# Kernel optimization log

Measured on AMD Instinct MI355X. Metric: run time of the kernel, lower is better.

The kernel has to match this reference:

```python
import jax, jax.numpy as jnp
import numpy as np

B, S, F, H, W = 16, 2048, 512, 512, 5
PAD = W // 2


def setup_inputs() -> dict:
    key = jax.random.key(0)
    k = jax.random.split(key, 6)
    scale = 0.02
    return {
        "embeds_output": jax.random.normal(k[0], (B, S, F), dtype=jnp.float32),
        "Wq": jax.random.normal(k[1], (F, H), dtype=jnp.float32) * scale,
        "Wk": jax.random.normal(k[2], (F, H), dtype=jnp.float32) * scale,
        "v_att": jax.random.normal(k[3], (H,), dtype=jnp.float32) * scale,
        "cnn_W": jax.random.normal(k[4], (W * F, H), dtype=jnp.float32) * scale,
        "cnn_b": jax.random.normal(k[5], (H,), dtype=jnp.float32) * scale,
    }


def reference(embeds_output, Wq, Wk, v_att, cnn_W, cnn_b):
    b, s, f = embeds_output.shape
    # getConvEmbeds: zero-pad and gather W shifted views -> [B, S, W, F]
    xp = jnp.pad(embeds_output, ((0, 0), (PAD, PAD), (0, 0)))
    windows = jnp.stack([xp[:, i:i + s, :] for i in range(W)], axis=2)  # [B,S,W,F]
    entity = windows[:, :, PAD, :]  # center token, [B,S,F]
    # Bahdanau additive attention over the window
    q = jnp.einsum('bsf,fh->bsh', entity, Wq)          # [B,S,H]
    kproj = jnp.einsum('bswf,fh->bswh', windows, Wk)   # [B,S,W,H]
    scores = jnp.einsum('bswh,h->bsw', jnp.tanh(kproj + q[:, :, None, :]), v_att)
    att = jax.nn.softmax(scores, axis=-1)              # [B,S,W]
    # weight contexts, flatten window dim (row-major W*F, matching torch reshape)
    att_context = (att[..., None] * windows).reshape(b, s, W * F)
    return att_context @ cnn_W + cnn_b                 # [B,S,H]
```

## Files before the change

### kernel.cpp

```cpp
#include <hip/hip_runtime.h>
#include <stdint.h>
#include <stddef.h>

typedef unsigned short u16;
typedef __attribute__((ext_vector_type(8))) short s16x8;
typedef __attribute__((ext_vector_type(8))) unsigned short u16x8;
typedef __attribute__((ext_vector_type(4))) unsigned short u16x4;
typedef __attribute__((ext_vector_type(4))) float f32x4;

typedef __attribute__((address_space(3))) void* as3_void_p;
typedef const __attribute__((address_space(1))) void* as1_cvoid_p;

#define GLD16(gp, lp) __builtin_amdgcn_global_load_lds((as1_cvoid_p)(gp), (as3_void_p)(lp), 16, 0, 0)

enum {
  NS = 2048, NF = 512, NH = 512, NW = 5,
  NROW = 32768,
  K2 = NW * NF
};

__device__ __forceinline__ u16 f2bf(float f) {
  unsigned u = __float_as_uint(f);
  u += 0x7FFFu + ((u >> 16) & 1u);
  return (u16)(u >> 16);
}
__device__ __forceinline__ float bf2f(u16 v) {
  return __uint_as_float(((unsigned)v) << 16);
}


__global__ __launch_bounds__(256) void cvtX(const float* __restrict__ X, u16* __restrict__ Xb) {
  int i = blockIdx.x * 256 + threadIdx.x;
  f32x4 v = ((const f32x4*)X)[i];
  u16x4 o;
  o.x = f2bf(v.x); o.y = f2bf(v.y); o.z = f2bf(v.z); o.w = f2bf(v.w);
  ((u16x4*)Xb)[i] = o;
}

__global__ __launch_bounds__(256) void cvtW(const float* __restrict__ Wq, const float* __restrict__ Wk,
                                            const float* __restrict__ cnnW,
                                            u16* __restrict__ Wt1, u16* __restrict__ Wt2) {
  int i = blockIdx.x * 256 + threadIdx.x;
  if (i < 1024 * 512) {
    int j = i >> 9, f = i & 511;
    float v = (j < 512) ? Wq[(size_t)f * 512 + j] : Wk[(size_t)f * 512 + (j - 512)];
    Wt1[i] = f2bf(v);
  } else {
    int t = i - 1024 * 512;
    int h = t / K2, k = t % K2;
    Wt2[t] = f2bf(cnnW[(size_t)k * 512 + h]);
  }
}


__global__ __launch_bounds__(256) void gemm_qk(const u16* __restrict__ Xb,
                                               const u16* __restrict__ Wt1,
                                               u16* __restrict__ QKb) {
  __shared__ u16 As[128 * 64];
  __shared__ u16 Bs[128 * 64];
  const int tid  = threadIdx.x;
  const int lane = tid & 63, wid = tid >> 6;
  const int wr = wid >> 1, wc = wid & 1;
  const int fr = lane & 15, fq = lane >> 4;
  const int wgid = (blockIdx.x & 7) * 256 + (blockIdx.x >> 3);
  const int brow = (wgid >> 3) * 128;
  const int bcol = (wgid & 7) * 128;

  f32x4 acc[4][4] = {};

  for (int kt = 0; kt < 8; ++kt) {
#pragma unroll
    for (int p = 0; p < 4; ++p) {
      int off = (p * 256 + tid) * 16;
      int r = off >> 7;
      int cb = (off & 127) ^ ((r & 7) << 4);
      const u16* ga = Xb  + (size_t)(brow + r) * NF + kt * 64 + (cb >> 1);
      const u16* gb = Wt1 + (size_t)(bcol + r) * NF + kt * 64 + (cb >> 1);
      GLD16(ga, (char*)As + off);
      GLD16(gb, (char*)Bs + off);
    }
    __syncthreads();
#pragma unroll
    for (int kk = 0; kk < 2; ++kk) {
      s16x8 af[4], bfr[4];
#pragma unroll
      for (int m = 0; m < 4; ++m) {
        int row = wr * 64 + m * 16 + fr;
        af[m] = *(const s16x8*)((const char*)As + row * 128 + ((kk * 64 + fq * 16) ^ ((row & 7) << 4)));
      }
#pragma unroll
      for (int n = 0; n < 4; ++n) {
        int row = wc * 64 + n * 16 + fr;
        bfr[n] = *(const s16x8*)((const char*)Bs + row * 128 + ((kk * 64 + fq * 16) ^ ((row & 7) << 4)));
      }
#pragma unroll
      for (int m = 0; m < 4; ++m)
#pragma unroll
        for (int n = 0; n < 4; ++n)
          acc[m][n] = __builtin_amdgcn_mfma_f32_16x16x32_bf16(af[m], bfr[n], acc[m][n], 0, 0, 0);
    }
    __syncthreads();
  }

#pragma unroll
  for (int m = 0; m < 4; ++m)
#pragma unroll
    for (int n = 0; n < 4; ++n)
#pragma unroll
      for (int r = 0; r < 4; ++r) {
        int row = brow + wr * 64 + m * 16 + fq * 4 + r;
        int col = bcol + wc * 64 + n * 16 + fr;
        QKb[(size_t)row * 1024 + col] = f2bf(acc[m][n][r]);
      }
}


__global__ __launch_bounds__(256) void scores_att(const u16* __restrict__ QKb,
                                                  const float* __restrict__ vatt,
                                                  float* __restrict__ att) {
  const int lane = threadIdx.x & 63;
  const int wid  = threadIdx.x >> 6;
  const int n = blockIdx.x * 4 + wid;
  const int s = n & (NS - 1);
  const int h0 = lane * 8;

  u16x8 qv = *(const u16x8*)(QKb + (size_t)n * 1024 + h0);
  f32x4 va0 = *(const f32x4*)(vatt + h0);
  f32x4 va1 = *(const f32x4*)(vatt + h0 + 4);
  float q[8], vv[8];
#pragma unroll
  for (int j = 0; j < 8; ++j) q[j] = bf2f(qv[j]);
  vv[0] = va0.x; vv[1] = va0.y; vv[2] = va0.z; vv[3] = va0.w;
  vv[4] = va1.x; vv[5] = va1.y; vv[6] = va1.z; vv[7] = va1.w;

  float sc[5];
#pragma unroll
  for (int w = 0; w < 5; ++w) {
    int sp = s + w - 2;
    u16x8 kv = {0, 0, 0, 0, 0, 0, 0, 0};
    if (sp >= 0 && sp < NS)
      kv = *(const u16x8*)(QKb + (size_t)(n + w - 2) * 1024 + 512 + h0);
    float acc = 0.f;
#pragma unroll
    for (int j = 0; j < 8; ++j) {
      float x = q[j] + bf2f(kv[j]);
      x = fminf(fmaxf(x, -15.f), 15.f);
      float e = __expf(2.f * x);
      acc += vv[j] * ((e - 1.f) / (e + 1.f));
    }
    sc[w] = acc;
  }
#pragma unroll
  for (int w = 0; w < 5; ++w)
#pragma unroll
    for (int o = 32; o > 0; o >>= 1)
      sc[w] += __shfl_xor(sc[w], o, 64);

  if (lane == 0) {
    float m = sc[0];
#pragma unroll
    for (int w = 1; w < 5; ++w) m = fmaxf(m, sc[w]);
    float e[5], sum = 0.f;
#pragma unroll
    for (int w = 0; w < 5; ++w) { e[w] = __expf(sc[w] - m); sum += e[w]; }
    float inv = 1.f / sum;
#pragma unroll
    for (int w = 0; w < 5; ++w) att[(size_t)n * 5 + w] = e[w] * inv;
  }
}


__global__ __launch_bounds__(512, 4) void gemm_out(const u16* __restrict__ Xb,
                                                   const u16* __restrict__ Wt2,
                                                   const float* __restrict__ att,
                                                   const float* __restrict__ cnnb,
                                                   float* __restrict__ out) {
  __shared__ u16 As[128 * 64];
  __shared__ u16 Bs[128 * 64];
  __shared__ float att_s[128 * 5];
  const int tid  = threadIdx.x;
  const int lane = tid & 63, wid = tid >> 6;
  const int wr = wid >> 2, wc = wid & 3;
  const int fr = lane & 15, fq = lane >> 4;
  const int wgid = (blockIdx.x & 7) * 128 + (blockIdx.x >> 3);
  const int brow = (wgid >> 2) * 128;
  const int bcol = (wgid & 3) * 128;

  if (tid < 128) {
    int s = (brow + tid) & (NS - 1);
#pragma unroll
    for (int w = 0; w < 5; ++w) {
      int sp = s + w - 2;
      att_s[tid * 5 + w] = (sp >= 0 && sp < NS) ? att[(size_t)(brow + tid) * 5 + w] : 0.f;
    }
  }

  const int rsub = tid >> 3;
  const int cb   = (((tid & 7) ^ (rsub & 7)) << 4);
  const int ldsA0 = tid * 16;
  const int ldsA1 = 8192 + tid * 16;
  const int ldsB0 = tid * 16;
  const int ldsB1 = 8192 + tid * 16;
  const char* gB0 = (const char*)(Wt2 + (size_t)(bcol + rsub) * K2) + cb;
  const char* gB1 = (const char*)(Wt2 + (size_t)(bcol + 64 + rsub) * K2) + cb;

  f32x4 acc[4][2] = {};
  f32x4 accOut[4][2] = {};

  for (int w = 0; w < 5; ++w) {
    int g0 = brow + rsub + w - 2;
    int g1 = brow + 64 + rsub + w - 2;
    g0 = g0 < 0 ? 0 : (g0 >= NROW ? NROW - 1 : g0);
    g1 = g1 < 0 ? 0 : (g1 >= NROW ? NROW - 1 : g1);
    const char* gA0 = (const char*)(Xb + (size_t)g0 * NF) + cb;
    const char* gA1 = (const char*)(Xb + (size_t)g1 * NF) + cb;
    const char* gBw0 = gB0 + w * 1024;
    const char* gBw1 = gB1 + w * 1024;

    for (int kt = 0; kt < 8; ++kt) {
      GLD16(gA0  + kt * 128, (char*)As + ldsA0);
      GLD16(gA1  + kt * 128, (char*)As + ldsA1);
      GLD16(gBw0 + kt * 128, (char*)Bs + ldsB0);
      GLD16(gBw1 + kt * 128, (char*)Bs + ldsB1);
      __syncthreads();
#pragma unroll
      for (int kk = 0; kk < 2; ++kk) {
        s16x8 af[4], bfr[2];
#pragma unroll
        for (int m = 0; m < 4; ++m) {
          int row = wr * 64 + m * 16 + fr;
          af[m] = *(const s16x8*)((const char*)As + row * 128 + ((kk * 64 + fq * 16) ^ ((row & 7) << 4)));
        }
#pragma unroll
        for (int n = 0; n < 2; ++n) {
          int row = wc * 32 + n * 16 + fr;
          bfr[n] = *(const s16x8*)((const char*)Bs + row * 128 + ((kk * 64 + fq * 16) ^ ((row & 7) << 4)));
        }
#pragma unroll
        for (int m = 0; m < 4; ++m)
#pragma unroll
          for (int n = 0; n < 2; ++n)
            acc[m][n] = __builtin_amdgcn_mfma_f32_16x16x32_bf16(af[m], bfr[n], acc[m][n], 0, 0, 0);
      }
      __syncthreads();
    }
#pragma unroll
    for (int m = 0; m < 4; ++m) {
      float a0 = att_s[(wr * 64 + m * 16 + fq * 4 + 0) * 5 + w];
      float a1 = att_s[(wr * 64 + m * 16 + fq * 4 + 1) * 5 + w];
      float a2 = att_s[(wr * 64 + m * 16 + fq * 4 + 2) * 5 + w];
      float a3 = att_s[(wr * 64 + m * 16 + fq * 4 + 3) * 5 + w];
#pragma unroll
      for (int n = 0; n < 2; ++n) {
        accOut[m][n][0] += a0 * acc[m][n][0];
        accOut[m][n][1] += a1 * acc[m][n][1];
        accOut[m][n][2] += a2 * acc[m][n][2];
        accOut[m][n][3] += a3 * acc[m][n][3];
        acc[m][n] = f32x4{0.f, 0.f, 0.f, 0.f};
      }
    }
  }

#pragma unroll
  for (int m = 0; m < 4; ++m)
#pragma unroll
    for (int n = 0; n < 2; ++n)
#pragma unroll
      for (int r = 0; r < 4; ++r) {
        int row = brow + wr * 64 + m * 16 + fq * 4 + r;
        int col = bcol + wc * 32 + n * 16 + fr;
        out[(size_t)row * NH + col] = accOut[m][n][r] + cnnb[col];
      }
}


extern "C" void kernel_launch(void* const* d_in, const int* in_sizes, int n_in,
                              void* d_out, int out_size, void* d_ws, size_t ws_size,
                              hipStream_t stream) {
  const float* X    = (const float*)d_in[0];
  const float* Wq   = (const float*)d_in[1];
  const float* Wk   = (const float*)d_in[2];
  const float* vatt = (const float*)d_in[3];
  const float* cnnW = (const float*)d_in[4];
  const float* cnnb = (const float*)d_in[5];
  float* out = (float*)d_out;

  char* ws = (char*)d_ws;
  u16*   Xb  = (u16*)ws;
  u16*   Wt1 = (u16*)(ws + 33554432);
  u16*   Wt2 = (u16*)(ws + 34603008);
  u16*   QKb = (u16*)(ws + 37224448);
  float* att = (float*)(ws + 104333312);

  cvtX<<<dim3(NROW * NF / 4 / 256), dim3(256), 0, stream>>>(X, Xb);
  cvtW<<<dim3((1024 * 512 + 512 * K2) / 256), dim3(256), 0, stream>>>(Wq, Wk, cnnW, Wt1, Wt2);
  gemm_qk<<<dim3(2048), dim3(256), 0, stream>>>(Xb, Wt1, QKb);
  scores_att<<<dim3(NROW / 4), dim3(256), 0, stream>>>(QKb, vatt, att);
  gemm_out<<<dim3(1024), dim3(512), 0, stream>>>(Xb, Wt2, att, cnnb, out);
}
```

Measured before the change: 208.7 us.

## Merge conversion kernels, widen QK GEMM to 512 threads, swizzle scores blocks

Merges the X and weight conversion kernels into a single launch to save one launch and its tail. Reworks the QK GEMM to use 512 threads per 128x128 tile, so each wave holds 4x2 accumulators instead of 4x4 and issues one global-to-LDS load per operand half per k-step. This targets higher occupancy and fewer registers per wave. Also remaps the scores kernel block index with an XCD-style swizzle, which may change L2 locality.

```diff
diff --git a/kernel.cpp b/kernel.cpp
--- a/kernel.cpp
+++ b/kernel.cpp
@@ -16,7 +16,10 @@
 enum {
   NS = 2048, NF = 512, NH = 512, NW = 5,
   NROW = 32768,
-  K2 = NW * NF
+  K2 = NW * NF,
+  XBLOCKS = NROW * NF / 4 / 256,
+  W_ELEMS = 1024 * 512 + 512 * K2,
+  WBLOCKS = (W_ELEMS + 255) / 256
 };
 
 __device__ __forceinline__ u16 f2bf(float f) {
@@ -29,74 +32,82 @@
 }
 
 
-__global__ __launch_bounds__(256) void cvtX(const float* __restrict__ X, u16* __restrict__ Xb) {
-  int i = blockIdx.x * 256 + threadIdx.x;
-  f32x4 v = ((const f32x4*)X)[i];
-  u16x4 o;
-  o.x = f2bf(v.x); o.y = f2bf(v.y); o.z = f2bf(v.z); o.w = f2bf(v.w);
-  ((u16x4*)Xb)[i] = o;
-}
-
-__global__ __launch_bounds__(256) void cvtW(const float* __restrict__ Wq, const float* __restrict__ Wk,
-                                            const float* __restrict__ cnnW,
-                                            u16* __restrict__ Wt1, u16* __restrict__ Wt2) {
-  int i = blockIdx.x * 256 + threadIdx.x;
-  if (i < 1024 * 512) {
-    int j = i >> 9, f = i & 511;
-    float v = (j < 512) ? Wq[(size_t)f * 512 + j] : Wk[(size_t)f * 512 + (j - 512)];
-    Wt1[i] = f2bf(v);
+__global__ __launch_bounds__(256) void cvt_all(const float* __restrict__ X,
+                                               const float* __restrict__ Wq,
+                                               const float* __restrict__ Wk,
+                                               const float* __restrict__ cnnW,
+                                               u16* __restrict__ Xb,
+                                               u16* __restrict__ Wt1,
+                                               u16* __restrict__ Wt2) {
+  int b = blockIdx.x;
+  if (b < XBLOCKS) {
+    int i = b * 256 + threadIdx.x;
+    f32x4 v = ((const f32x4*)X)[i];
+    u16x4 o;
+    o.x = f2bf(v.x); o.y = f2bf(v.y); o.z = f2bf(v.z); o.w = f2bf(v.w);
+    ((u16x4*)Xb)[i] = o;
   } else {
-    int t = i - 1024 * 512;
-    int h = t / K2, k = t % K2;
-    Wt2[t] = f2bf(cnnW[(size_t)k * 512 + h]);
-  }
-}
-
-
-__global__ __launch_bounds__(256) void gemm_qk(const u16* __restrict__ Xb,
-                                               const u16* __restrict__ Wt1,
-                                               u16* __restrict__ QKb) {
+    int i = (b - XBLOCKS) * 256 + threadIdx.x;
+    if (i >= W_ELEMS) return;
+    if (i < 1024 * 512) {
+      int j = i >> 9, f = i & 511;
+      float v = (j < 512) ? Wq[(size_t)f * 512 + j] : Wk[(size_t)f * 512 + (j - 512)];
+      Wt1[i] = f2bf(v);
+    } else {
+      int t = i - 1024 * 512;
+      int h = t / K2, k = t % K2;
+      Wt2[t] = f2bf(cnnW[(size_t)k * 512 + h]);
+    }
+  }
+}
+
+
+__global__ __launch_bounds__(512, 4) void gemm_qk(const u16* __restrict__ Xb,
+                                                  const u16* __restrict__ Wt1,
+                                                  u16* __restrict__ QKb) {
   __shared__ u16 As[128 * 64];
   __shared__ u16 Bs[128 * 64];
   const int tid  = threadIdx.x;
   const int lane = tid & 63, wid = tid >> 6;
-  const int wr = wid >> 1, wc = wid & 1;
+  const int wr = wid >> 2, wc = wid & 3;
   const int fr = lane & 15, fq = lane >> 4;
   const int wgid = (blockIdx.x & 7) * 256 + (blockIdx.x >> 3);
   const int brow = (wgid >> 3) * 128;
   const int bcol = (wgid & 7) * 128;
 
-  f32x4 acc[4][4] = {};
+  const int rsub = tid >> 3;
+  const int cb   = (((tid & 7) ^ (rsub & 7)) << 4);
+  const char* gA0 = (const char*)(Xb  + (size_t)(brow + rsub) * NF) + cb;
+  const char* gA1 = (const char*)(Xb  + (size_t)(brow + 64 + rsub) * NF) + cb;
+  const char* gB0 = (const char*)(Wt1 + (size_t)(bcol + rsub) * NF) + cb;
+  const char* gB1 = (const char*)(Wt1 + (size_t)(bcol + 64 + rsub) * NF) + cb;
+
+  f32x4 acc[4][2] = {};
 
   for (int kt = 0; kt < 8; ++kt) {
-#pragma unroll
-    for (int p = 0; p < 4; ++p) {
-      int off = (p * 256 + tid) * 16;
-      int r = off >> 7;
-      int cb = (off & 127) ^ ((r & 7) << 4);
-      const u16* ga = Xb  + (size_t)(brow + r) * NF + kt * 64 + (cb >> 1);
-      const u16* gb = Wt1 + (size_t)(bcol + r) * NF + kt * 64 + (cb >> 1);
-      GLD16(ga, (char*)As + off);
-      GLD16(gb, (char*)Bs + off);
-    }
+    const int ko = kt * 128;
+    GLD16(gA0 + ko, (char*)As + tid * 16);
+    GLD16(gA1 + ko, (char*)As + 8192 + tid * 16);
+    GLD16(gB0 + ko, (char*)Bs + tid * 16);
+    GLD16(gB1 + ko, (char*)Bs + 8192 + tid * 16);
     __syncthreads();
 #pragma unroll
     for (int kk = 0; kk < 2; ++kk) {
-      s16x8 af[4], bfr[4];
+      s16x8 af[4], bfr[2];
 #pragma unroll
       for (int m = 0; m < 4; ++m) {
         int row = wr * 64 + m * 16 + fr;
         af[m] = *(const s16x8*)((const char*)As + row * 128 + ((kk * 64 + fq * 16) ^ ((row & 7) << 4)));
       }
 #pragma unroll
-      for (int n = 0; n < 4; ++n) {
-        int row = wc * 64 + n * 16 + fr;
+      for (int n = 0; n < 2; ++n) {
+        int row = wc * 32 + n * 16 + fr;
         bfr[n] = *(const s16x8*)((const char*)Bs + row * 128 + ((kk * 64 + fq * 16) ^ ((row & 7) << 4)));
       }
 #pragma unroll
       for (int m = 0; m < 4; ++m)
 #pragma unroll
-        for (int n = 0; n < 4; ++n)
+        for (int n = 0; n < 2; ++n)
           acc[m][n] = __builtin_amdgcn_mfma_f32_16x16x32_bf16(af[m], bfr[n], acc[m][n], 0, 0, 0);
     }
     __syncthreads();
@@ -105,11 +116,11 @@
 #pragma unroll
   for (int m = 0; m < 4; ++m)
 #pragma unroll
-    for (int n = 0; n < 4; ++n)
+    for (int n = 0; n < 2; ++n)
 #pragma unroll
       for (int r = 0; r < 4; ++r) {
         int row = brow + wr * 64 + m * 16 + fq * 4 + r;
-        int col = bcol + wc * 64 + n * 16 + fr;
+        int col = bcol + wc * 32 + n * 16 + fr;
         QKb[(size_t)row * 1024 + col] = f2bf(acc[m][n][r]);
       }
 }
@@ -120,7 +131,8 @@
                                                   float* __restrict__ att) {
   const int lane = threadIdx.x & 63;
   const int wid  = threadIdx.x >> 6;
-  const int n = blockIdx.x * 4 + wid;
+  const int wgid = (blockIdx.x & 7) * 1024 + (blockIdx.x >> 3);
+  const int n = wgid * 4 + wid;
   const int s = n & (NS - 1);
   const int h0 = lane * 8;
 
@@ -197,10 +209,6 @@
 
   const int rsub = tid >> 3;
   const int cb   = (((tid & 7) ^ (rsub & 7)) << 4);
-  const int ldsA0 = tid * 16;
-  const int ldsA1 = 8192 + tid * 16;
-  const int ldsB0 = tid * 16;
-  const int ldsB1 = 8192 + tid * 16;
   const char* gB0 = (const char*)(Wt2 + (size_t)(bcol + rsub) * K2) + cb;
   const char* gB1 = (const char*)(Wt2 + (size_t)(bcol + 64 + rsub) * K2) + cb;
 
@@ -218,10 +226,11 @@
     const char* gBw1 = gB1 + w * 1024;
 
     for (int kt = 0; kt < 8; ++kt) {
-      GLD16(gA0  + kt * 128, (char*)As + ldsA0);
-      GLD16(gA1  + kt * 128, (char*)As + ldsA1);
-      GLD16(gBw0 + kt * 128, (char*)Bs + ldsB0);
-      GLD16(gBw1 + kt * 128, (char*)Bs + ldsB1);
+      const int ko = kt * 128;
+      GLD16(gA0  + ko, (char*)As + tid * 16);
+      GLD16(gA1  + ko, (char*)As + 8192 + tid * 16);
+      GLD16(gBw0 + ko, (char*)Bs + tid * 16);
+      GLD16(gBw1 + ko, (char*)Bs + 8192 + tid * 16);
       __syncthreads();
 #pragma unroll
       for (int kk = 0; kk < 2; ++kk) {
@@ -292,9 +301,8 @@
   u16*   QKb = (u16*)(ws + 37224448);
   float* att = (float*)(ws + 104333312);
 
-  cvtX<<<dim3(NROW * NF / 4 / 256), dim3(256), 0, stream>>>(X, Xb);
-  cvtW<<<dim3((1024 * 512 + 512 * K2) / 256), dim3(256), 0, stream>>>(Wq, Wk, cnnW, Wt1, Wt2);
-  gemm_qk<<<dim3(2048), dim3(256), 0, stream>>>(Xb, Wt1, QKb);
+  cvt_all<<<dim3(XBLOCKS + WBLOCKS), dim3(256), 0, stream>>>(X, Wq, Wk, cnnW, Xb, Wt1, Wt2);
+  gemm_qk<<<dim3(2048), dim3(512), 0, stream>>>(Xb, Wt1, QKb);
   scores_att<<<dim3(NROW / 4), dim3(256), 0, stream>>>(QKb, vatt, att);
   gemm_out<<<dim3(1024), dim3(512), 0, stream>>>(Xb, Wt2, att, cnnb, out);
 }
```

Result: faster. 202.0 us (-3.2%).
